# Kernel tuning notes

Measured on AMD Instinct MI355X. Metric: run time of the kernel, lower is better.

The kernel has to match this reference:

```python
import jax, jax.numpy as jnp
import numpy as np

B, S, D = 2, 2048, 2560
H, DH = 32, 80           # heads, head_size = D // H
RD = 32                  # rotary_dim (partial RoPE)
NI = 10240               # n_inner = 4 * n_embd
EPS = 1e-5
ROPE_BASE = 10000.0


def setup_inputs() -> dict:
    key = jax.random.key(0)
    ks = jax.random.split(key, 12)
    sd = 0.02
    inp = {
        "position_ids": jnp.broadcast_to(jnp.arange(S, dtype=jnp.int64), (B, S)),
        "hidden_states": jax.random.normal(ks[0], (B, S, D), jnp.float32),
        "ln_g": jnp.ones((D,), jnp.float32),
        "ln_b": jnp.zeros((D,), jnp.float32),
        "wqkv": jax.random.normal(ks[1], (D, 3 * D), jnp.float32) * sd,
        "bqkv": jnp.zeros((3 * D,), jnp.float32),
        "wout": jax.random.normal(ks[2], (D, D), jnp.float32) * sd,
        "bout": jnp.zeros((D,), jnp.float32),
        "wfc1": jax.random.normal(ks[3], (D, NI), jnp.float32) * sd,
        "bfc1": jnp.zeros((NI,), jnp.float32),
        "wfc2": jax.random.normal(ks[4], (NI, D), jnp.float32) * sd,
        "bfc2": jnp.zeros((D,), jnp.float32),
    }
    return inp


def _rope_neox(x, positions):
    # x: [B,S,H,DH]; apply neox-style rotary to first RD dims only
    half = RD // 2
    inv_freq = 1.0 / (ROPE_BASE ** (jnp.arange(0, RD, 2, dtype=jnp.float32) / RD))  # [half]
    ang = positions.astype(jnp.float32)[..., None] * inv_freq                        # [B,S,half]
    cos = jnp.cos(ang)[:, :, None, :]  # [B,S,1,half]
    sin = jnp.sin(ang)[:, :, None, :]
    x1 = x[..., :half]
    x2 = x[..., half:RD]
    rot = jnp.concatenate([x1 * cos - x2 * sin, x2 * cos + x1 * sin], axis=-1)
    return jnp.concatenate([rot, x[..., RD:]], axis=-1)


def reference(position_ids, hidden_states, ln_g, ln_b, wqkv, bqkv, wout, bout,
              wfc1, bfc1, wfc2, bfc2):
    residual = hidden_states
    # LayerNorm
    mu = jnp.mean(hidden_states, axis=-1, keepdims=True)
    var = jnp.mean(jnp.square(hidden_states - mu), axis=-1, keepdims=True)
    x = (hidden_states - mu) * jax.lax.rsqrt(var + EPS) * ln_g + ln_b

    # QKV projection
    qkv = x @ wqkv + bqkv
    q, k, v = jnp.split(qkv, 3, axis=-1)
    q = q.reshape(B, S, H, DH)
    k = k.reshape(B, S, H, DH)
    v = v.reshape(B, S, H, DH)

    # partial RoPE (neox style) on q and k
    q = _rope_neox(q, position_ids)
    k = _rope_neox(k, position_ids)

    # causal attention
    scale = DH ** -0.5
    scores = jnp.einsum("bqhd,bkhd->bhqk", q, k) * scale
    causal = jnp.tril(jnp.ones((S, S), jnp.bool_))
    scores = jnp.where(causal, scores, jnp.finfo(scores.dtype).min)
    probs = jax.nn.softmax(scores, axis=-1)
    attn = jnp.einsum("bhqk,bkhd->bqhd", probs, v).reshape(B, S, D)
    attn_out = attn @ wout + bout

    # MLP (gelu_new = tanh-approx gelu) on the SAME normed x (parallel residual)
    mlp = jax.nn.gelu(x @ wfc1 + bfc1, approximate=True) @ wfc2 + bfc2

    return attn_out + mlp + residual
```

## Files before the change

kernel.cpp:

```cpp
#include <hip/hip_runtime.h>

#define SS   2048
#define DD   2560
#define HH   32
#define DHH  80
#define DPAD 96
#define NII  10240
#define NTOK 4096

typedef __attribute__((ext_vector_type(8))) __bf16 bf16x8;
typedef __attribute__((ext_vector_type(4))) float  f32x4;

__device__ __forceinline__ float bf2f(unsigned short h) {
  union { unsigned u; float f; } c; c.u = ((unsigned)h) << 16; return c.f;
}
__device__ __forceinline__ unsigned short f2bf(float f) {
  union { float f; unsigned u; } c; c.f = f;
  unsigned r = c.u + 0x7FFFu + ((c.u >> 16) & 1u);
  return (unsigned short)(r >> 16);
}

__device__ __forceinline__ void gl_lds16(const void* gptr, void* lptr) {
  __builtin_amdgcn_global_load_lds((__attribute__((address_space(1))) void*)gptr,
                                   (__attribute__((address_space(3))) void*)lptr,
                                   16, 0, 0);
}

__global__ __launch_bounds__(256) void wt_transpose(const float* __restrict__ W,
                                                    unsigned short* __restrict__ Wt,
                                                    int K, int N) {
  __shared__ float tile[32][33];
  const int tx = threadIdx.x & 31, ty = threadIdx.x >> 5;
  const int n0 = blockIdx.x * 32, k0 = blockIdx.y * 32;
#pragma unroll
  for (int i = 0; i < 32; i += 8)
    tile[ty + i][tx] = W[(size_t)(k0 + ty + i) * N + n0 + tx];
  __syncthreads();
#pragma unroll
  for (int i = 0; i < 32; i += 8)
    Wt[(size_t)(n0 + ty + i) * K + k0 + tx] = f2bf(tile[tx][ty + i]);
}

__global__ __launch_bounds__(256) void ln_kernel(const float* __restrict__ X,
                                                 const float* __restrict__ G,
                                                 const float* __restrict__ Bb,
                                                 unsigned short* __restrict__ Xo) {
  const int row = blockIdx.x;
  const float4* xr = (const float4*)(X + (size_t)row * DD);
  float s = 0.f, ss = 0.f;
  for (int i = threadIdx.x; i < DD / 4; i += 256) {
    float4 v = xr[i];
    s  += v.x + v.y + v.z + v.w;
    ss += v.x * v.x + v.y * v.y + v.z * v.z + v.w * v.w;
  }
#pragma unroll
  for (int o = 32; o > 0; o >>= 1) { s += __shfl_down(s, o, 64); ss += __shfl_down(ss, o, 64); }
  __shared__ float red[8];
  const int w = threadIdx.x >> 6;
  if ((threadIdx.x & 63) == 0) { red[w] = s; red[4 + w] = ss; }
  __syncthreads();
  if (threadIdx.x == 0) {
    float ts  = red[0] + red[1] + red[2] + red[3];
    float tss = red[4] + red[5] + red[6] + red[7];
    float mu  = ts * (1.f / DD);
    float var = tss * (1.f / DD) - mu * mu;
    red[0] = mu; red[1] = rsqrtf(var + 1e-5f);
  }
  __syncthreads();
  const float mu = red[0], rstd = red[1];
  const float4* gr = (const float4*)G;
  const float4* br = (const float4*)Bb;
  for (int i = threadIdx.x; i < DD / 4; i += 256) {
    float4 v = xr[i], g = gr[i], b = br[i];
    ushort4 o;
    o.x = f2bf((v.x - mu) * rstd * g.x + b.x);
    o.y = f2bf((v.y - mu) * rstd * g.y + b.y);
    o.z = f2bf((v.z - mu) * rstd * g.z + b.z);
    o.w = f2bf((v.w - mu) * rstd * g.w + b.w);
    *(ushort4*)&Xo[(size_t)row * DD + i * 4] = o;
  }
}

__global__ __launch_bounds__(256) void rope_kernel(const unsigned short* __restrict__ qkv,
                                                   unsigned short* __restrict__ Qp,
                                                   unsigned short* __restrict__ Kp,
                                                   unsigned short* __restrict__ Vt) {
  const int tok = blockIdx.x;
  const int b = tok / SS, s = tok % SS;
  __shared__ float cs[16], sn[16];
  if (threadIdx.x < 16) {
    float inv = powf(10000.f, -(float)threadIdx.x / 16.f);
    float ang = (float)s * inv;
    cs[threadIdx.x] = cosf(ang);
    sn[threadIdx.x] = sinf(ang);
  }
  __syncthreads();
  const unsigned short* row = qkv + (size_t)tok * (3 * DD);
  for (int idx = threadIdx.x; idx < 2 * HH * DPAD; idx += 256) {
    const int which = idx / (HH * DPAD);
    const int rrem  = idx % (HH * DPAD);
    const int h = rrem / DPAD, d = rrem % DPAD;
    float val = 0.f;
    if (d < DHH) {
      const unsigned short* base = row + which * DD + h * DHH;
      if (d < 16) {
        float x1 = bf2f(base[d]), x2 = bf2f(base[d + 16]);
        val = x1 * cs[d] - x2 * sn[d];
      } else if (d < 32) {
        int i2 = d - 16;
        float x1 = bf2f(base[i2]), x2 = bf2f(base[d]);
        val = x2 * cs[i2] + x1 * sn[i2];
      } else {
        val = bf2f(base[d]);
      }
    }
    unsigned short* outp = which ? Kp : Qp;
    outp[(((size_t)b * HH + h) * SS + s) * DPAD + d] = f2bf(val);
  }
  for (int idx = threadIdx.x; idx < DD; idx += 256) {
    const int h = idx / DHH, d = idx % DHH;
    Vt[(((size_t)b * HH + h) * DHH + d) * SS + s] = row[2 * DD + idx];
  }
}

__global__ __launch_bounds__(128) void attn_kernel(const unsigned short* __restrict__ Qp,
                                                   const unsigned short* __restrict__ Kp,
                                                   const unsigned short* __restrict__ Vt,
                                                   unsigned short* __restrict__ O) {
  const int bid = blockIdx.x;
  const int bh = bid & 63;
  const int p = 31 - (bid >> 6);
  const int w = threadIdx.x >> 6;
  const int tile = p * 2 + w;
  const int lane = threadIdx.x & 63;
  const int lr = lane & 15, lg = lane >> 4;
  const int q0 = tile * 32;
  const unsigned short* Qh = Qp + (size_t)bh * SS * DPAD;
  const unsigned short* Kh = Kp + (size_t)bh * SS * DPAD;
  const unsigned short* Vh = Vt + (size_t)bh * DHH * SS;
  __shared__ __align__(16) char Plds[2][2][2048];

  bf16x8 qf[2][3];
#pragma unroll
  for (int g = 0; g < 2; ++g)
#pragma unroll
    for (int c = 0; c < 3; ++c)
      qf[g][c] = *(const bf16x8*)&Qh[(size_t)(q0 + g * 16 + lr) * DPAD + c * 32 + lg * 8];

  f32x4 oacc[2][5];
#pragma unroll
  for (int g = 0; g < 2; ++g)
#pragma unroll
    for (int d = 0; d < 5; ++d) oacc[g][d] = (f32x4){0.f, 0.f, 0.f, 0.f};
  float mrow[2][4], lrow[2][4];
#pragma unroll
  for (int g = 0; g < 2; ++g)
#pragma unroll
    for (int r = 0; r < 4; ++r) { mrow[g][r] = -1e30f; lrow[g][r] = 0.f; }

  const float scl = 0.11180339887498949f;
  const int nt = (q0 + 31) / 64 + 1;
  for (int t = 0; t < nt; ++t) {
    const int kv0 = t * 64;
    f32x4 s[2][4];
#pragma unroll
    for (int g = 0; g < 2; ++g)
#pragma unroll
      for (int j = 0; j < 4; ++j) s[g][j] = (f32x4){0.f, 0.f, 0.f, 0.f};
#pragma unroll
    for (int c = 0; c < 3; ++c) {
      bf16x8 kf[4];
#pragma unroll
      for (int j = 0; j < 4; ++j)
        kf[j] = *(const bf16x8*)&Kh[(size_t)(kv0 + j * 16 + lr) * DPAD + c * 32 + lg * 8];
#pragma unroll
      for (int g = 0; g < 2; ++g)
#pragma unroll
        for (int j = 0; j < 4; ++j)
          s[g][j] = __builtin_amdgcn_mfma_f32_16x16x32_bf16(qf[g][c], kf[j], s[g][j], 0, 0, 0);
    }
    float pv[2][4][4], mx[2][4];
    bool need = false;
#pragma unroll
    for (int g = 0; g < 2; ++g) {
#pragma unroll
      for (int r = 0; r < 4; ++r) {
        const int qr = q0 + g * 16 + lg * 4 + r;
        float m = -1e30f;
#pragma unroll
        for (int j = 0; j < 4; ++j) {
          float a = (kv0 + j * 16 + lr > qr) ? -1e30f : s[g][j][r] * scl;
          pv[g][j][r] = a;
          m = fmaxf(m, a);
        }
#pragma unroll
        for (int mk = 1; mk < 16; mk <<= 1) m = fmaxf(m, __shfl_xor(m, mk, 64));
        mx[g][r] = m;
        need = need || (m > mrow[g][r] + 8.f);
      }
    }
    if (__ballot(need)) {
#pragma unroll
      for (int g = 0; g < 2; ++g)
#pragma unroll
        for (int r = 0; r < 4; ++r) {
          float mnew = fmaxf(mrow[g][r], mx[g][r]);
          float resc = __expf(mrow[g][r] - mnew);
          lrow[g][r] *= resc;
#pragma unroll
          for (int d = 0; d < 5; ++d) oacc[g][d][r] *= resc;
          mrow[g][r] = mnew;
        }
    }
#pragma unroll
    for (int g = 0; g < 2; ++g) {
      char* Pb = Plds[w][g];
#pragma unroll
      for (int r = 0; r < 4; ++r) {
        const int row = lg * 4 + r;
        const int swz = (row & 7) << 4;
        float rs = 0.f;
#pragma unroll
        for (int j = 0; j < 4; ++j) {
          float pj = __expf(pv[g][j][r] - mrow[g][r]);
          rs += pj;
          *(unsigned short*)(Pb + row * 128 + (((j * 16 + lr) * 2) ^ swz)) = f2bf(pj);
        }
#pragma unroll
        for (int mk = 1; mk < 16; mk <<= 1) rs += __shfl_xor(rs, mk, 64);
        lrow[g][r] += rs;
      }
    }
    asm volatile("s_waitcnt lgkmcnt(0)" ::: "memory");
    const int rswz = (lr & 7) << 4;
    bf16x8 pa[2][2];
#pragma unroll
    for (int g = 0; g < 2; ++g) {
      pa[g][0] = *(const bf16x8*)(Plds[w][g] + lr * 128 + ((lg * 16) ^ rswz));
      pa[g][1] = *(const bf16x8*)(Plds[w][g] + lr * 128 + ((64 + lg * 16) ^ rswz));
    }
#pragma unroll
    for (int d = 0; d < 5; ++d) {
      bf16x8 v0 = *(const bf16x8*)&Vh[(size_t)(d * 16 + lr) * SS + kv0 + lg * 8];
      bf16x8 v1 = *(const bf16x8*)&Vh[(size_t)(d * 16 + lr) * SS + kv0 + 32 + lg * 8];
#pragma unroll
      for (int g = 0; g < 2; ++g) {
        oacc[g][d] = __builtin_amdgcn_mfma_f32_16x16x32_bf16(pa[g][0], v0, oacc[g][d], 0, 0, 0);
        oacc[g][d] = __builtin_amdgcn_mfma_f32_16x16x32_bf16(pa[g][1], v1, oacc[g][d], 0, 0, 0);
      }
    }
  }
  const int b = bh >> 5, h = bh & 31;
#pragma unroll
  for (int g = 0; g < 2; ++g)
#pragma unroll
    for (int r = 0; r < 4; ++r) {
      const int qr = q0 + g * 16 + lg * 4 + r;
      const float inv = 1.f / lrow[g][r];
#pragma unroll
      for (int d = 0; d < 5; ++d)
        O[(size_t)(b * SS + qr) * DD + h * DHH + d * 16 + lr] = f2bf(oacc[g][d][r] * inv);
    }
}

__device__ __forceinline__ float gelu_f(float x) {
  float x3 = x * x * x;
  return 0.5f * x * (1.f + tanhf(0.7978845608028654f * (x + 0.044715f * x3)));
}

template <int MODE>
__global__ __launch_bounds__(512, 2) void gemm256(const unsigned short* __restrict__ A,
                                                  const unsigned short* __restrict__ Bt,
                                                  const float* __restrict__ bias,
                                                  void* __restrict__ Cout,
                                                  const unsigned short* __restrict__ addb,
                                                  const float* __restrict__ addf,
                                                  int M, int N, int K, int nby) {
  __shared__ __align__(16) char lds[131072];

  const int bid = blockIdx.x;
  const int by = bid % nby, bx = bid / nby;
  const int m0 = by * 256, n0 = bx * 256;

  const int tid = threadIdx.x;
  const int w = tid >> 6, lane = tid & 63;
  const int lr = lane & 15, lg = lane >> 4;
  const int wm = w >> 2, wn = w & 3;

  const int srow = w * 16 + (lane >> 3);
  const int scol = ((lane & 7) ^ ((lane >> 3) & 7)) * 8;
  const unsigned short* pA = A  + (size_t)(m0 + srow) * K + scol;
  const unsigned short* pB = Bt + (size_t)(n0 + srow) * K + scol;
  const int wdst = w * 2048;

  const int rdA = wm * 16384 + lr * 128;
  const int rdB = 65536 + (wn >> 1) * 16384 + ((wn & 1) * 64 + lr) * 128;
  const int sl0 = ((lg) ^ (lr & 7)) << 4;
  const int sl1 = ((4 + lg) ^ (lr & 7)) << 4;

  f32x4 acc[8][4];
#pragma unroll
  for (int i = 0; i < 8; ++i)
#pragma unroll
    for (int j = 0; j < 4; ++j) acc[i][j] = (f32x4){0.f, 0.f, 0.f, 0.f};

  const int nt = K >> 6;

#define RA(BUF, m, kh) (*(const bf16x8*)(lds + (BUF) + rdA + (m) * 2048 + ((kh) ? sl1 : sl0)))
#define RB(BUF, n, kh) (*(const bf16x8*)(lds + (BUF) + rdB + (n) * 2048 + ((kh) ? sl1 : sl0)))
#define STGA(dt, h, DST)                                                       \
  { const unsigned short* s_ = pA + (size_t)(dt) * 64 + (size_t)(h) * 128 * K; \
    gl_lds16(s_,                 lds + (DST) + wdst);                          \
    gl_lds16(s_ + (size_t)8 * K, lds + (DST) + wdst + 1024); }
#define STGB(dt, h, DST)                                                       \
  { const unsigned short* s_ = pB + (size_t)(dt) * 64 + (size_t)(h) * 128 * K; \
    gl_lds16(s_,                 lds + 65536 + (DST) + wdst);                  \
    gl_lds16(s_ + (size_t)8 * K, lds + 65536 + (DST) + wdst + 1024); }
#define BARR __builtin_amdgcn_s_barrier()
#define MFMA8x2(AV, BV, MB, NB)                                              \
  __builtin_amdgcn_s_setprio(1);                                             \
  _Pragma("unroll") for (int kh_ = 0; kh_ < 2; ++kh_)                        \
  _Pragma("unroll") for (int m_ = 0; m_ < 4; ++m_)                           \
  _Pragma("unroll") for (int n_ = 0; n_ < 2; ++n_)                           \
    acc[(MB) + m_][(NB) + n_] = __builtin_amdgcn_mfma_f32_16x16x32_bf16(     \
        AV[m_][kh_], BV[n_][kh_], acc[(MB) + m_][(NB) + n_], 0, 0, 0);       \
  __builtin_amdgcn_s_setprio(0);

  STGA(0, 0, 0);
  STGA(0, 1, 16384);
  STGB(0, 0, 0);
  STGB(0, 1, 16384);
  STGA(1, 0, 32768);
  STGA(1, 1, 32768 + 16384);
  STGB(1, 0, 32768);
  asm volatile("s_waitcnt vmcnt(6)" ::: "memory");
  BARR;
  __builtin_amdgcn_sched_barrier(0);

  for (int t = 0; t < nt; t += 2) {
    const bool more = (t + 2 < nt);
    bf16x8 avL[4][2], avH[4][2], bvL[2][2], bvH[2][2];

#pragma unroll
    for (int m_ = 0; m_ < 4; ++m_) { avL[m_][0] = RA(0, m_, 0); avL[m_][1] = RA(0, m_, 1); }
#pragma unroll
    for (int n_ = 0; n_ < 2; ++n_) { bvL[n_][0] = RB(0, n_, 0); bvL[n_][1] = RB(0, n_, 1); }
    STGB(1, 1, 32768 + 16384);
    BARR;
    MFMA8x2(avL, bvL, 0, 0);
    BARR;
#pragma unroll
    for (int m_ = 0; m_ < 4; ++m_) { avH[m_][0] = RA(0, 4 + m_, 0); avH[m_][1] = RA(0, 4 + m_, 1); }
    BARR;
    MFMA8x2(avH, bvL, 4, 0);
    BARR;
#pragma unroll
    for (int n_ = 0; n_ < 2; ++n_) { bvH[n_][0] = RB(0, 2 + n_, 0); bvH[n_][1] = RB(0, 2 + n_, 1); }
    if (more) STGA(2, 0, 0);
    BARR;
    MFMA8x2(avH, bvH, 4, 2);
    BARR;
    if (more) STGA(2, 1, 16384);
    BARR;
    MFMA8x2(avL, bvH, 0, 2);
    if (more) { asm volatile("s_waitcnt vmcnt(4)" ::: "memory"); }
    else      { asm volatile("s_waitcnt vmcnt(0)" ::: "memory"); }
    BARR;
    __builtin_amdgcn_sched_barrier(0);

#pragma unroll
    for (int m_ = 0; m_ < 4; ++m_) { avL[m_][0] = RA(32768, m_, 0); avL[m_][1] = RA(32768, m_, 1); }
#pragma unroll
    for (int n_ = 0; n_ < 2; ++n_) { bvL[n_][0] = RB(32768, n_, 0); bvL[n_][1] = RB(32768, n_, 1); }
    if (more) STGB(2, 0, 0);
    BARR;
    MFMA8x2(avL, bvL, 0, 0);
    BARR;
#pragma unroll
    for (int m_ = 0; m_ < 4; ++m_) { avH[m_][0] = RA(32768, 4 + m_, 0); avH[m_][1] = RA(32768, 4 + m_, 1); }
    if (more) STGB(2, 1, 16384);
    BARR;
    MFMA8x2(avH, bvL, 4, 0);
    BARR;
#pragma unroll
    for (int n_ = 0; n_ < 2; ++n_) { bvH[n_][0] = RB(32768, 2 + n_, 0); bvH[n_][1] = RB(32768, 2 + n_, 1); }
    if (more) STGA(3, 0, 32768);
    BARR;
    MFMA8x2(avH, bvH, 4, 2);
    BARR;
    if (more) { STGA(3, 1, 32768 + 16384); STGB(3, 0, 32768); }
    BARR;
    MFMA8x2(avL, bvH, 0, 2);
    if (more) { asm volatile("s_waitcnt vmcnt(6)" ::: "memory"); }
    BARR;
    __builtin_amdgcn_sched_barrier(0);

    pA += 128; pB += 128;
  }
#undef RA
#undef RB
#undef STGA
#undef STGB
#undef BARR
#undef MFMA8x2

#pragma unroll
  for (int m = 0; m < 8; ++m) {
    const int rb = m0 + wm * 128 + m * 16 + lg * 4;
#pragma unroll
    for (int n = 0; n < 4; ++n) {
      const int col = n0 + wn * 64 + n * 16 + lr;
      const float bv = bias[col];
#pragma unroll
      for (int r = 0; r < 4; ++r) {
        const size_t idx = (size_t)(rb + r) * N + col;
        float v = acc[m][n][r] + bv;
        if (MODE == 2) v = gelu_f(v);
        if (MODE == 3) {
          ((float*)Cout)[idx] = v + bf2f(addb[idx]) + addf[idx];
        } else {
          ((unsigned short*)Cout)[idx] = f2bf(v);
        }
      }
    }
  }
}

extern "C" void kernel_launch(void* const* d_in, const int* in_sizes, int n_in,
                              void* d_out, int out_size, void* d_ws, size_t ws_size,
                              hipStream_t stream) {
  (void)in_sizes; (void)n_in; (void)out_size; (void)ws_size;
  const float* hidden = (const float*)d_in[1];
  const float* ln_g = (const float*)d_in[2];
  const float* ln_b = (const float*)d_in[3];
  const float* wqkv = (const float*)d_in[4];
  const float* bqkv = (const float*)d_in[5];
  const float* wout = (const float*)d_in[6];
  const float* bout = (const float*)d_in[7];
  const float* wfc1 = (const float*)d_in[8];
  const float* bfc1 = (const float*)d_in[9];
  const float* wfc2 = (const float*)d_in[10];
  const float* bfc2 = (const float*)d_in[11];
  float* out = (float*)d_out;

  char* ws = (char*)d_ws;
  size_t off = 0;
  auto alloc = [&](size_t bytes) -> void* {
    void* p = ws + off;
    off += (bytes + 255) & ~(size_t)255;
    return p;
  };
  unsigned short* wqkvT = (unsigned short*)alloc((size_t)3 * DD * DD * 2);
  unsigned short* woutT = (unsigned short*)alloc((size_t)DD * DD * 2);
  unsigned short* wfc1T = (unsigned short*)alloc((size_t)NII * DD * 2);
  unsigned short* wfc2T = (unsigned short*)alloc((size_t)DD * NII * 2);
  unsigned short* xln   = (unsigned short*)alloc((size_t)NTOK * DD * 2);
  unsigned short* regA  = (unsigned short*)alloc((size_t)NTOK * NII * 2);
  unsigned short* Qp    = (unsigned short*)alloc((size_t)2 * HH * SS * DPAD * 2);
  unsigned short* Kp    = (unsigned short*)alloc((size_t)2 * HH * SS * DPAD * 2);
  unsigned short* Vt    = (unsigned short*)alloc((size_t)2 * HH * DHH * SS * 2);
  unsigned short* Obuf  = (unsigned short*)alloc((size_t)NTOK * DD * 2);
  unsigned short* qkvbuf   = regA;
  unsigned short* h1       = regA;
  unsigned short* attnproj = Qp;

  wt_transpose<<<dim3(3 * DD / 32, DD / 32), 256, 0, stream>>>(wqkv, wqkvT, DD, 3 * DD);
  wt_transpose<<<dim3(DD / 32, DD / 32), 256, 0, stream>>>(wout, woutT, DD, DD);
  wt_transpose<<<dim3(NII / 32, DD / 32), 256, 0, stream>>>(wfc1, wfc1T, DD, NII);
  wt_transpose<<<dim3(DD / 32, NII / 32), 256, 0, stream>>>(wfc2, wfc2T, NII, DD);
  ln_kernel<<<NTOK, 256, 0, stream>>>(hidden, ln_g, ln_b, xln);
  gemm256<0><<<dim3((3 * DD / 256) * (NTOK / 256)), 512, 0, stream>>>(
      xln, wqkvT, bqkv, qkvbuf, nullptr, nullptr, NTOK, 3 * DD, DD, NTOK / 256);
  rope_kernel<<<NTOK, 256, 0, stream>>>(qkvbuf, Qp, Kp, Vt);
  attn_kernel<<<dim3(2048), 128, 0, stream>>>(Qp, Kp, Vt, Obuf);
  gemm256<0><<<dim3((DD / 256) * (NTOK / 256)), 512, 0, stream>>>(
      Obuf, woutT, bout, attnproj, nullptr, nullptr, NTOK, DD, DD, NTOK / 256);
  gemm256<2><<<dim3((NII / 256) * (NTOK / 256)), 512, 0, stream>>>(
      xln, wfc1T, bfc1, h1, nullptr, nullptr, NTOK, NII, DD, NTOK / 256);
  gemm256<3><<<dim3((DD / 256) * (NTOK / 256)), 512, 0, stream>>>(
      h1, wfc2T, bfc2, out, attnproj, hidden, NTOK, DD, NII, NTOK / 256);
}
```

Before: 1.220 ms.

## Split-K the fc2 GEMM into two halves with a separate reduction kernel

The fc2 GEMM (K=10240) now runs as two K-halves, using twice as many 256x256 tile blocks. This targets the original 160-block grid, which left many CUs idle. Each half writes fp32 partials into the start of the workspace, where the already-consumed transposed weights lived. A new elementwise kernel then sums the partials and adds bias, the attention projection and the residual. The cost is roughly 84MB of extra fp32 partial writes and reads, plus one more launch.

New measurement: 1.263 ms. +3.5%, slower.

```diff
diff --git a/kernel.cpp b/kernel.cpp
--- a/kernel.cpp
+++ b/kernel.cpp
@@ -275,11 +275,14 @@
                                                   void* __restrict__ Cout,
                                                   const unsigned short* __restrict__ addb,
                                                   const float* __restrict__ addf,
-                                                  int M, int N, int K, int nby) {
+                                                  int M, int N, int K, int nby,
+                                                  int Kcnt, int tps) {
   __shared__ __align__(16) char lds[131072];
 
   const int bid = blockIdx.x;
-  const int by = bid % nby, bx = bid / nby;
+  const int s = bid / tps;
+  const int inner = bid % tps;
+  const int by = inner % nby, bx = inner / nby;
   const int m0 = by * 256, n0 = bx * 256;
 
   const int tid = threadIdx.x;
@@ -289,8 +292,8 @@
 
   const int srow = w * 16 + (lane >> 3);
   const int scol = ((lane & 7) ^ ((lane >> 3) & 7)) * 8;
-  const unsigned short* pA = A  + (size_t)(m0 + srow) * K + scol;
-  const unsigned short* pB = Bt + (size_t)(n0 + srow) * K + scol;
+  const unsigned short* pA = A  + (size_t)(m0 + srow) * K + scol + (size_t)s * Kcnt;
+  const unsigned short* pB = Bt + (size_t)(n0 + srow) * K + scol + (size_t)s * Kcnt;
   const int wdst = w * 2048;
 
   const int rdA = wm * 16384 + lr * 128;
@@ -304,7 +307,7 @@
 #pragma unroll
     for (int j = 0; j < 4; ++j) acc[i][j] = (f32x4){0.f, 0.f, 0.f, 0.f};
 
-  const int nt = K >> 6;
+  const int nt = Kcnt >> 6;
 
 #define RA(BUF, m, kh) (*(const bf16x8*)(lds + (BUF) + rdA + (m) * 2048 + ((kh) ? sl1 : sl0)))
 #define RB(BUF, n, kh) (*(const bf16x8*)(lds + (BUF) + rdB + (n) * 2048 + ((kh) ? sl1 : sl0)))
@@ -404,13 +407,14 @@
 #undef BARR
 #undef MFMA8x2
 
+  float* pdst = (MODE == 4) ? ((float*)Cout + (size_t)s * M * N) : (float*)Cout;
 #pragma unroll
   for (int m = 0; m < 8; ++m) {
     const int rb = m0 + wm * 128 + m * 16 + lg * 4;
 #pragma unroll
     for (int n = 0; n < 4; ++n) {
       const int col = n0 + wn * 64 + n * 16 + lr;
-      const float bv = bias[col];
+      const float bv = (MODE == 4) ? 0.f : bias[col];
 #pragma unroll
       for (int r = 0; r < 4; ++r) {
         const size_t idx = (size_t)(rb + r) * N + col;
@@ -418,11 +422,36 @@
         if (MODE == 2) v = gelu_f(v);
         if (MODE == 3) {
           ((float*)Cout)[idx] = v + bf2f(addb[idx]) + addf[idx];
+        } else if (MODE == 4) {
+          pdst[idx] = v;
         } else {
           ((unsigned short*)Cout)[idx] = f2bf(v);
         }
       }
     }
+  }
+}
+
+__global__ __launch_bounds__(256) void fc2_reduce(const float* __restrict__ P0,
+                                                  const float* __restrict__ P1,
+                                                  const float* __restrict__ bias,
+                                                  const unsigned short* __restrict__ addb,
+                                                  const float* __restrict__ addf,
+                                                  float* __restrict__ out) {
+  const size_t total = (size_t)NTOK * DD / 4;
+  for (size_t i = (size_t)blockIdx.x * 256 + threadIdx.x; i < total; i += (size_t)gridDim.x * 256) {
+    float4 a = ((const float4*)P0)[i];
+    float4 b = ((const float4*)P1)[i];
+    const int col = (int)((i * 4) % DD);
+    float4 bi = *(const float4*)&bias[col];
+    ushort4 ab = ((const ushort4*)addb)[i];
+    float4 af = ((const float4*)addf)[i];
+    float4 r;
+    r.x = a.x + b.x + bi.x + bf2f(ab.x) + af.x;
+    r.y = a.y + b.y + bi.y + bf2f(ab.y) + af.y;
+    r.z = a.z + b.z + bi.z + bf2f(ab.z) + af.z;
+    r.w = a.w + b.w + bi.w + bf2f(ab.w) + af.w;
+    ((float4*)out)[i] = r;
   }
 }
 
@@ -463,20 +492,35 @@
   unsigned short* qkvbuf   = regA;
   unsigned short* h1       = regA;
   unsigned short* attnproj = Qp;
+  float* fc2part = (float*)ws;
 
   wt_transpose<<<dim3(3 * DD / 32, DD / 32), 256, 0, stream>>>(wqkv, wqkvT, DD, 3 * DD);
   wt_transpose<<<dim3(DD / 32, DD / 32), 256, 0, stream>>>(wout, woutT, DD, DD);
   wt_transpose<<<dim3(NII / 32, DD / 32), 256, 0, stream>>>(wfc1, wfc1T, DD, NII);
   wt_transpose<<<dim3(DD / 32, NII / 32), 256, 0, stream>>>(wfc2, wfc2T, NII, DD);
   ln_kernel<<<NTOK, 256, 0, stream>>>(hidden, ln_g, ln_b, xln);
-  gemm256<0><<<dim3((3 * DD / 256) * (NTOK / 256)), 512, 0, stream>>>(
-      xln, wqkvT, bqkv, qkvbuf, nullptr, nullptr, NTOK, 3 * DD, DD, NTOK / 256);
+  {
+    const int tps = (3 * DD / 256) * (NTOK / 256);
+    gemm256<0><<<dim3(tps), 512, 0, stream>>>(
+        xln, wqkvT, bqkv, qkvbuf, nullptr, nullptr, NTOK, 3 * DD, DD, NTOK / 256, DD, tps);
+  }
   rope_kernel<<<NTOK, 256, 0, stream>>>(qkvbuf, Qp, Kp, Vt);
   attn_kernel<<<dim3(2048), 128, 0, stream>>>(Qp, Kp, Vt, Obuf);
-  gemm256<0><<<dim3((DD / 256) * (NTOK / 256)), 512, 0, stream>>>(
-      Obuf, woutT, bout, attnproj, nullptr, nullptr, NTOK, DD, DD, NTOK / 256);
-  gemm256<2><<<dim3((NII / 256) * (NTOK / 256)), 512, 0, stream>>>(
-      xln, wfc1T, bfc1, h1, nullptr, nullptr, NTOK, NII, DD, NTOK / 256);
-  gemm256<3><<<dim3((DD / 256) * (NTOK / 256)), 512, 0, stream>>>(
-      h1, wfc2T, bfc2, out, attnproj, hidden, NTOK, DD, NII, NTOK / 256);
-}
+  {
+    const int tps = (DD / 256) * (NTOK / 256);
+    gemm256<0><<<dim3(tps), 512, 0, stream>>>(
+        Obuf, woutT, bout, attnproj, nullptr, nullptr, NTOK, DD, DD, NTOK / 256, DD, tps);
+  }
+  {
+    const int tps = (NII / 256) * (NTOK / 256);
+    gemm256<2><<<dim3(tps), 512, 0, stream>>>(
+        xln, wfc1T, bfc1, h1, nullptr, nullptr, NTOK, NII, DD, NTOK / 256, DD, tps);
+  }
+  {
+    const int tps = (DD / 256) * (NTOK / 256);
+    gemm256<4><<<dim3(2 * tps), 512, 0, stream>>>(
+        h1, wfc2T, nullptr, fc2part, nullptr, nullptr, NTOK, DD, NII, NTOK / 256, NII / 2, tps);
+  }
+  fc2_reduce<<<dim3(2048), 256, 0, stream>>>(
+      fc2part, fc2part + (size_t)NTOK * DD, bfc2, attnproj, hidden, out);
+}
```
